# Optimization experiments

Hardware: AMD Instinct MI355X
Metric: run time of the kernel (lower is better)

## Reference

```python
import jax, jax.numpy as jnp
import numpy as np

MARGIN = 1.0


def setup_inputs() -> dict:
    key = jax.random.key(0)
    k1, k2 = jax.random.split(key)
    embeddings = jax.random.normal(k1, (4096, 512), dtype=jnp.float32)
    labels = jax.random.randint(k2, (4096,), 0, 256, dtype=jnp.int32)
    return {"embeddings": embeddings, "labels": labels}


def _masked_random_gather(dist, mask, key):
    # Uniformly sample one valid (masked-True) column per row via argmax of
    # uniform noise restricted to the mask (equivalent to torch.randint over
    # the per-row index list, fully vectorized). Rows with no valid entry -> 0.
    B = dist.shape[0]
    u = jax.random.uniform(key, mask.shape)          # [B, B] in [0, 1)
    idx = jnp.argmax(jnp.where(mask, u, -1.0), axis=1)  # [B]
    has_valid = jnp.any(mask, axis=1)
    d = dist[jnp.arange(B), idx]
    return jnp.where(has_valid, d, 0.0)


def reference(embeddings, labels):
    B = embeddings.shape[0]
    # Pairwise squared Euclidean distances: ||a||^2 + ||b||^2 - 2 a.b, clamped >= 0
    dot = embeddings @ embeddings.T                  # [B, B]
    sq = jnp.diagonal(dot)                           # [B]
    dist = jax.nn.relu(sq[None, :] + sq[:, None] - 2.0 * dot)

    same = labels[:, None] == labels[None, :]        # [B, B]
    eye = jnp.eye(B, dtype=bool)
    mask_pos = same & ~eye
    mask_neg = ~same

    kp, kn = jax.random.split(jax.random.key(42))
    positive_dist = _masked_random_gather(dist, mask_pos, kp)
    negative_dist = _masked_random_gather(dist, mask_neg, kn)

    triplet_loss = jax.nn.relu(positive_dist - negative_dist + MARGIN)
    valid = jnp.sum(triplet_loss > 1e-16)
    return jnp.where(valid == 0, jnp.float32(0.0), jnp.mean(triplet_loss))
```

## Files before the change

kernel.cpp:

```cpp
#include <hip/hip_runtime.h>
#include <stdint.h>

#define B 4096
#define D 512

#define NB_POS 16
#define NB_SQ 64
#define NB_NEG 2048
#define NB_TOTAL (NB_POS + NB_SQ + NB_NEG)

__host__ __device__ __forceinline__ uint32_t rotl32(uint32_t x, int d) {
#ifdef __HIP_DEVICE_COMPILE__
    return __builtin_amdgcn_alignbit(x, x, (uint32_t)(32 - d));
#else
    return (x << d) | (x >> (32 - d));
#endif
}

__host__ __device__ __forceinline__ void tf2x32(uint32_t k0, uint32_t k1,
                                                uint32_t x0, uint32_t x1,
                                                uint32_t& o0, uint32_t& o1) {
    const uint32_t k2 = k0 ^ k1 ^ 0x1BD11BDAu;
#define TF_ROUND(r) { x0 += x1; x1 = rotl32(x1, r); x1 ^= x0; }
    x0 += k0; x1 += k1;
    TF_ROUND(13) TF_ROUND(15) TF_ROUND(26) TF_ROUND(6)
    x0 += k1; x1 += k2 + 1u;
    TF_ROUND(17) TF_ROUND(29) TF_ROUND(16) TF_ROUND(24)
    x0 += k2; x1 += k0 + 2u;
    TF_ROUND(13) TF_ROUND(15) TF_ROUND(26) TF_ROUND(6)
    x0 += k0; x1 += k1 + 3u;
    TF_ROUND(17) TF_ROUND(29) TF_ROUND(16) TF_ROUND(24)
    x0 += k1; x1 += k2 + 4u;
    TF_ROUND(13) TF_ROUND(15) TF_ROUND(26) TF_ROUND(6)
    x0 += k2; x1 += k0 + 5u;
#undef TF_ROUND
    o0 = x0; o1 = x1;
}

__device__ __forceinline__ uint32_t draw32(uint32_t k0, uint32_t k1,
                                           uint32_t flat) {
    uint32_t o0, o1;
    tf2x32(k0, k1, 0u, flat, o0, o1);
    return o0 ^ o1;
}

__device__ __forceinline__ unsigned long long umax64(unsigned long long a,
                                                     unsigned long long b) {
    return a > b ? a : b;
}

__device__ __forceinline__ unsigned long long packbest(int bestv, int bestc) {
    return (bestv < 0)
               ? 0ull
               : ((((unsigned long long)(uint32_t)bestv + 1ull) << 12) |
                  (unsigned long long)(uint32_t)(4095 - bestc));
}

__global__ __launch_bounds__(256) void fused_select_kernel(
        const float* __restrict__ E, const int* __restrict__ labels,
        float* __restrict__ sq, int* __restrict__ idxp, int* __restrict__ idxn,
        uint32_t kp0, uint32_t kp1, uint32_t kn0, uint32_t kn1) {
    __shared__ unsigned short bposc[B];
    __shared__ int cnt[256];
    __shared__ int basex[256];
    __shared__ int fillc[256];
    __shared__ unsigned long long red[2][4];

    const int bid = blockIdx.x;
    const int t = threadIdx.x;
    const int lane = t & 63;
    const int w = t >> 6;

    if (bid >= NB_POS + NB_SQ) {
        const int r0 = (bid - (NB_POS + NB_SQ)) * 2;
        const int4* lp = (const int4*)(labels + (t << 4));
        const int4 La = lp[0], Lb = lp[1], Lc = lp[2], Ld = lp[3];
        const int lab16[16] = {La.x, La.y, La.z, La.w, Lb.x, Lb.y, Lb.z, Lb.w,
                               Lc.x, Lc.y, Lc.z, Lc.w, Ld.x, Ld.y, Ld.z, Ld.w};
        const int labr0 = labels[r0];
        const int labr1 = labels[r0 + 1];
        const uint32_t f0 = ((uint32_t)r0 << 12) + ((uint32_t)t << 4);
        int bv0 = -1, bc0 = 0, bv1 = -1, bc1 = 0;
#pragma unroll
        for (int j = 0; j < 16; ++j) {
            const int c = (t << 4) + j;
            const uint32_t h0 = draw32(kn0, kn1, f0 + (uint32_t)j);
            const uint32_t h1 = draw32(kn0, kn1, f0 + (uint32_t)j + 4096u);
            const int v0 = (int)(h0 >> 9);
            const int v1 = (int)(h1 >> 9);
            if ((lab16[j] != labr0) & (v0 > bv0)) { bv0 = v0; bc0 = c; }
            if ((lab16[j] != labr1) & (v1 > bv1)) { bv1 = v1; bc1 = c; }
        }
        unsigned long long p0 = packbest(bv0, bc0);
        unsigned long long p1 = packbest(bv1, bc1);
#pragma unroll
        for (int off = 32; off > 0; off >>= 1) {
            p0 = umax64(p0, __shfl_down(p0, off));
            p1 = umax64(p1, __shfl_down(p1, off));
        }
        if (lane == 0) { red[0][w] = p0; red[1][w] = p1; }
        __syncthreads();
        if (t < 2) {
            unsigned long long best = red[t][0];
#pragma unroll
            for (int k = 1; k < 4; ++k) best = umax64(best, red[t][k]);
            idxn[r0 + t] = best ? (int)(4095u - (uint32_t)(best & 0xFFFull))
                                : -1;
        }
    } else if (bid < NB_POS) {
        const int4* lp = (const int4*)(labels + (t << 4));
        const int4 La = lp[0], Lb = lp[1], Lc = lp[2], Ld = lp[3];
        const int lab16[16] = {La.x, La.y, La.z, La.w, Lb.x, Lb.y, Lb.z, Lb.w,
                               Lc.x, Lc.y, Lc.z, Lc.w, Ld.x, Ld.y, Ld.z, Ld.w};
        cnt[t] = 0;
        fillc[t] = 0;
        __syncthreads();
#pragma unroll
        for (int j = 0; j < 16; ++j) atomicAdd(&cnt[lab16[j]], 1);
        __syncthreads();
        basex[t] = cnt[t];
        __syncthreads();
        for (int off = 1; off < 256; off <<= 1) {
            const int u = (t >= off) ? basex[t - off] : 0;
            __syncthreads();
            basex[t] += u;
            __syncthreads();
        }
#pragma unroll
        for (int j = 0; j < 16; ++j) {
            const int l = lab16[j];
            const int off = atomicAdd(&fillc[l], 1);
            bposc[basex[l] - cnt[l] + off] = (unsigned short)((t << 4) + j);
        }
        __syncthreads();
        const int r = bid * 256 + t;
        const int myl = labels[r];
        const int s1 = basex[myl];
        const int s0 = s1 - cnt[myl];
        const uint32_t rbase = (uint32_t)r << 12;
        unsigned long long best = 0ull;
        for (int i = s0; i < s1; ++i) {
            const int c = (int)bposc[i];
            if (c == r) continue;
            const uint32_t bits = draw32(kp0, kp1, rbase + (uint32_t)c);
            const unsigned long long pack =
                ((((unsigned long long)(bits >> 9)) + 1ull) << 12) |
                (unsigned long long)(uint32_t)(4095 - c);
            best = umax64(best, pack);
        }
        idxp[r] = best ? (int)(4095u - (uint32_t)(best & 0xFFFull)) : -1;
    } else {
        const int base = (bid - NB_POS) * 64 + w * 16;
#pragma unroll 2
        for (int k = 0; k < 16; ++k) {
            const int r = base + k;
            const float4* er = (const float4*)(E + (size_t)r * D);
            float4 a0 = er[lane * 2];
            float4 a1 = er[lane * 2 + 1];
            float s = a0.x * a0.x + a0.y * a0.y + a0.z * a0.z + a0.w * a0.w +
                      a1.x * a1.x + a1.y * a1.y + a1.z * a1.z + a1.w * a1.w;
#pragma unroll
            for (int off = 32; off > 0; off >>= 1) s += __shfl_down(s, off);
            if (lane == 0) sq[r] = s;
        }
    }
}

__global__ __launch_bounds__(256) void loss_kernel(
        const float* __restrict__ E, const float* __restrict__ sq,
        const int* __restrict__ idxp, const int* __restrict__ idxn,
        float* __restrict__ tl) {
    const int lane = threadIdx.x & 63;
    const int w = threadIdx.x >> 6;
    const int r = blockIdx.x * 4 + w;
    const int ip = idxp[r];
    const int in_ = idxn[r];
    const float4* er = (const float4*)(E + (size_t)r * D);
    float dp = 0.f, dn = 0.f;
    float4 a0 = er[lane * 2];
    float4 a1 = er[lane * 2 + 1];
    if (ip >= 0) {
        const float4* ep = (const float4*)(E + (size_t)ip * D);
        float4 b0 = ep[lane * 2];
        float4 b1 = ep[lane * 2 + 1];
        dp = a0.x * b0.x + a0.y * b0.y + a0.z * b0.z + a0.w * b0.w +
             a1.x * b1.x + a1.y * b1.y + a1.z * b1.z + a1.w * b1.w;
    }
    if (in_ >= 0) {
        const float4* en = (const float4*)(E + (size_t)in_ * D);
        float4 b0 = en[lane * 2];
        float4 b1 = en[lane * 2 + 1];
        dn = a0.x * b0.x + a0.y * b0.y + a0.z * b0.z + a0.w * b0.w +
             a1.x * b1.x + a1.y * b1.y + a1.z * b1.z + a1.w * b1.w;
    }
#pragma unroll
    for (int off = 32; off > 0; off >>= 1) {
        dp += __shfl_down(dp, off);
        dn += __shfl_down(dn, off);
    }
    if (lane == 0) {
        const float pd = (ip >= 0) ? fmaxf(sq[r] + sq[ip] - 2.0f * dp, 0.f) : 0.f;
        const float nd = (in_ >= 0) ? fmaxf(sq[r] + sq[in_] - 2.0f * dn, 0.f) : 0.f;
        tl[r] = fmaxf(pd - nd + 1.0f, 0.f);
    }
}

__global__ __launch_bounds__(256) void finalize_kernel(
        const float* __restrict__ tl, float* __restrict__ out) {
    const int t = threadIdx.x;
    float s = 0.f;
    int c = 0;
    for (int j = t; j < B; j += 256) {
        const float v = tl[j];
        s += v;
        if (v > 1e-16f) c++;
    }
#pragma unroll
    for (int off = 32; off > 0; off >>= 1) {
        s += __shfl_down(s, off);
        c += __shfl_down(c, off);
    }
    __shared__ float ss[4];
    __shared__ int sc[4];
    if ((t & 63) == 0) { ss[t >> 6] = s; sc[t >> 6] = c; }
    __syncthreads();
    if (t == 0) {
#pragma unroll
        for (int k = 1; k < 4; ++k) { s += ss[k]; c += sc[k]; }
        out[0] = (c == 0) ? 0.0f : s * (1.0f / 4096.0f);
    }
}

extern "C" void kernel_launch(void* const* d_in, const int* in_sizes, int n_in,
                              void* d_out, int out_size, void* d_ws,
                              size_t ws_size, hipStream_t stream) {
    const float* E = (const float*)d_in[0];
    const int* labels = (const int*)d_in[1];
    float* out = (float*)d_out;

    char* ws = (char*)d_ws;
    float* sq = (float*)(ws);
    int* idxp = (int*)(ws + 16384);
    int* idxn = (int*)(ws + 32768);
    float* tl = (float*)(ws + 49152);

    uint32_t kp0, kp1, kn0, kn1;
    tf2x32(0u, 42u, 0u, 0u, kp0, kp1);
    tf2x32(0u, 42u, 0u, 1u, kn0, kn1);

    fused_select_kernel<<<NB_TOTAL, 256, 0, stream>>>(E, labels, sq, idxp,
                                                      idxn, kp0, kp1, kn0, kn1);
    loss_kernel<<<B / 4, 256, 0, stream>>>(E, sq, idxp, idxn, tl);
    finalize_kernel<<<1, 256, 0, stream>>>(tl, out);
}
```

Measured before the change: 50.07 us.

## Move positive selection and squared norms into loss kernel, publish label buckets

```diff
diff --git a/kernel.cpp b/kernel.cpp
--- a/kernel.cpp
+++ b/kernel.cpp
@@ -4,10 +4,7 @@
 #define B 4096
 #define D 512
 
-#define NB_POS 16
-#define NB_SQ 64
 #define NB_NEG 2048
-#define NB_TOTAL (NB_POS + NB_SQ + NB_NEG)
 
 __host__ __device__ __forceinline__ uint32_t rotl32(uint32_t x, int d) {
 #ifdef __HIP_DEVICE_COMPILE__
@@ -56,11 +53,10 @@
                   (unsigned long long)(uint32_t)(4095 - bestc));
 }
 
-__global__ __launch_bounds__(256) void fused_select_kernel(
-        const float* __restrict__ E, const int* __restrict__ labels,
-        float* __restrict__ sq, int* __restrict__ idxp, int* __restrict__ idxn,
-        uint32_t kp0, uint32_t kp1, uint32_t kn0, uint32_t kn1) {
-    __shared__ unsigned short bposc[B];
+__global__ __launch_bounds__(256) void neg_bucket_kernel(
+        const int* __restrict__ labels, int* __restrict__ idxn,
+        int* __restrict__ bstart, unsigned short* __restrict__ bcols,
+        uint32_t kn0, uint32_t kn1) {
     __shared__ int cnt[256];
     __shared__ int basex[256];
     __shared__ int fillc[256];
@@ -71,43 +67,7 @@
     const int lane = t & 63;
     const int w = t >> 6;
 
-    if (bid >= NB_POS + NB_SQ) {
-        const int r0 = (bid - (NB_POS + NB_SQ)) * 2;
-        const int4* lp = (const int4*)(labels + (t << 4));
-        const int4 La = lp[0], Lb = lp[1], Lc = lp[2], Ld = lp[3];
-        const int lab16[16] = {La.x, La.y, La.z, La.w, Lb.x, Lb.y, Lb.z, Lb.w,
-                               Lc.x, Lc.y, Lc.z, Lc.w, Ld.x, Ld.y, Ld.z, Ld.w};
-        const int labr0 = labels[r0];
-        const int labr1 = labels[r0 + 1];
-        const uint32_t f0 = ((uint32_t)r0 << 12) + ((uint32_t)t << 4);
-        int bv0 = -1, bc0 = 0, bv1 = -1, bc1 = 0;
-#pragma unroll
-        for (int j = 0; j < 16; ++j) {
-            const int c = (t << 4) + j;
-            const uint32_t h0 = draw32(kn0, kn1, f0 + (uint32_t)j);
-            const uint32_t h1 = draw32(kn0, kn1, f0 + (uint32_t)j + 4096u);
-            const int v0 = (int)(h0 >> 9);
-            const int v1 = (int)(h1 >> 9);
-            if ((lab16[j] != labr0) & (v0 > bv0)) { bv0 = v0; bc0 = c; }
-            if ((lab16[j] != labr1) & (v1 > bv1)) { bv1 = v1; bc1 = c; }
-        }
-        unsigned long long p0 = packbest(bv0, bc0);
-        unsigned long long p1 = packbest(bv1, bc1);
-#pragma unroll
-        for (int off = 32; off > 0; off >>= 1) {
-            p0 = umax64(p0, __shfl_down(p0, off));
-            p1 = umax64(p1, __shfl_down(p1, off));
-        }
-        if (lane == 0) { red[0][w] = p0; red[1][w] = p1; }
-        __syncthreads();
-        if (t < 2) {
-            unsigned long long best = red[t][0];
-#pragma unroll
-            for (int k = 1; k < 4; ++k) best = umax64(best, red[t][k]);
-            idxn[r0 + t] = best ? (int)(4095u - (uint32_t)(best & 0xFFFull))
-                                : -1;
-        }
-    } else if (bid < NB_POS) {
+    if (bid == 0) {
         const int4* lp = (const int4*)(labels + (t << 4));
         const int4 La = lp[0], Lb = lp[1], Lc = lp[2], Ld = lp[3];
         const int lab16[16] = {La.x, La.y, La.z, La.w, Lb.x, Lb.y, Lb.z, Lb.w,
@@ -126,81 +86,117 @@
             basex[t] += u;
             __syncthreads();
         }
+        bstart[t] = basex[t] - cnt[t];
+        if (t == 255) bstart[256] = B;
 #pragma unroll
         for (int j = 0; j < 16; ++j) {
             const int l = lab16[j];
             const int off = atomicAdd(&fillc[l], 1);
-            bposc[basex[l] - cnt[l] + off] = (unsigned short)((t << 4) + j);
+            bcols[basex[l] - cnt[l] + off] = (unsigned short)((t << 4) + j);
         }
         __syncthreads();
-        const int r = bid * 256 + t;
-        const int myl = labels[r];
-        const int s1 = basex[myl];
-        const int s0 = s1 - cnt[myl];
-        const uint32_t rbase = (uint32_t)r << 12;
-        unsigned long long best = 0ull;
-        for (int i = s0; i < s1; ++i) {
-            const int c = (int)bposc[i];
-            if (c == r) continue;
-            const uint32_t bits = draw32(kp0, kp1, rbase + (uint32_t)c);
-            const unsigned long long pack =
-                ((((unsigned long long)(bits >> 9)) + 1ull) << 12) |
-                (unsigned long long)(uint32_t)(4095 - c);
-            best = umax64(best, pack);
-        }
-        idxp[r] = best ? (int)(4095u - (uint32_t)(best & 0xFFFull)) : -1;
-    } else {
-        const int base = (bid - NB_POS) * 64 + w * 16;
-#pragma unroll 2
-        for (int k = 0; k < 16; ++k) {
-            const int r = base + k;
-            const float4* er = (const float4*)(E + (size_t)r * D);
-            float4 a0 = er[lane * 2];
-            float4 a1 = er[lane * 2 + 1];
-            float s = a0.x * a0.x + a0.y * a0.y + a0.z * a0.z + a0.w * a0.w +
-                      a1.x * a1.x + a1.y * a1.y + a1.z * a1.z + a1.w * a1.w;
-#pragma unroll
-            for (int off = 32; off > 0; off >>= 1) s += __shfl_down(s, off);
-            if (lane == 0) sq[r] = s;
-        }
+    }
+
+    const int r0 = bid * 2;
+    const int4* lp = (const int4*)(labels + (t << 4));
+    const int4 La = lp[0], Lb = lp[1], Lc = lp[2], Ld = lp[3];
+    const int lab16[16] = {La.x, La.y, La.z, La.w, Lb.x, Lb.y, Lb.z, Lb.w,
+                           Lc.x, Lc.y, Lc.z, Lc.w, Ld.x, Ld.y, Ld.z, Ld.w};
+    const int labr0 = labels[r0];
+    const int labr1 = labels[r0 + 1];
+    const uint32_t f0 = ((uint32_t)r0 << 12) + ((uint32_t)t << 4);
+    int bv0 = -1, bc0 = 0, bv1 = -1, bc1 = 0;
+#pragma unroll
+    for (int j = 0; j < 16; ++j) {
+        const int c = (t << 4) + j;
+        const uint32_t h0 = draw32(kn0, kn1, f0 + (uint32_t)j);
+        const uint32_t h1 = draw32(kn0, kn1, f0 + (uint32_t)j + 4096u);
+        const int v0 = (int)(h0 >> 9);
+        const int v1 = (int)(h1 >> 9);
+        if ((lab16[j] != labr0) & (v0 > bv0)) { bv0 = v0; bc0 = c; }
+        if ((lab16[j] != labr1) & (v1 > bv1)) { bv1 = v1; bc1 = c; }
+    }
+    unsigned long long p0 = packbest(bv0, bc0);
+    unsigned long long p1 = packbest(bv1, bc1);
+#pragma unroll
+    for (int off = 32; off > 0; off >>= 1) {
+        p0 = umax64(p0, __shfl_down(p0, off));
+        p1 = umax64(p1, __shfl_down(p1, off));
+    }
+    if (lane == 0) { red[0][w] = p0; red[1][w] = p1; }
+    __syncthreads();
+    if (t < 2) {
+        unsigned long long best = red[t][0];
+#pragma unroll
+        for (int k = 1; k < 4; ++k) best = umax64(best, red[t][k]);
+        idxn[r0 + t] = best ? (int)(4095u - (uint32_t)(best & 0xFFFull)) : -1;
     }
 }
 
 __global__ __launch_bounds__(256) void loss_kernel(
-        const float* __restrict__ E, const float* __restrict__ sq,
-        const int* __restrict__ idxp, const int* __restrict__ idxn,
-        float* __restrict__ tl) {
+        const float* __restrict__ E, const int* __restrict__ labels,
+        const int* __restrict__ bstart, const unsigned short* __restrict__ bcols,
+        const int* __restrict__ idxn, float* __restrict__ tl,
+        uint32_t kp0, uint32_t kp1) {
     const int lane = threadIdx.x & 63;
     const int w = threadIdx.x >> 6;
     const int r = blockIdx.x * 4 + w;
-    const int ip = idxp[r];
+
+    const int l = labels[r];
+    const int s0 = bstart[l];
+    const int s1 = bstart[l + 1];
+    const uint32_t rbase = (uint32_t)r << 12;
+    unsigned long long best = 0ull;
+    for (int i = s0 + lane; i < s1; i += 64) {
+        const int c = (int)bcols[i];
+        if (c == r) continue;
+        const uint32_t bits = draw32(kp0, kp1, rbase + (uint32_t)c);
+        const unsigned long long pack =
+            ((((unsigned long long)(bits >> 9)) + 1ull) << 12) |
+            (unsigned long long)(uint32_t)(4095 - c);
+        best = umax64(best, pack);
+    }
+#pragma unroll
+    for (int off = 32; off > 0; off >>= 1)
+        best = umax64(best, __shfl_xor(best, off));
+    const int ip = best ? (int)(4095u - (uint32_t)(best & 0xFFFull)) : -1;
     const int in_ = idxn[r];
+
     const float4* er = (const float4*)(E + (size_t)r * D);
-    float dp = 0.f, dn = 0.f;
     float4 a0 = er[lane * 2];
     float4 a1 = er[lane * 2 + 1];
+    float aa = a0.x * a0.x + a0.y * a0.y + a0.z * a0.z + a0.w * a0.w +
+               a1.x * a1.x + a1.y * a1.y + a1.z * a1.z + a1.w * a1.w;
+    float dp = 0.f, pp = 0.f, dn = 0.f, nn = 0.f;
     if (ip >= 0) {
         const float4* ep = (const float4*)(E + (size_t)ip * D);
         float4 b0 = ep[lane * 2];
         float4 b1 = ep[lane * 2 + 1];
         dp = a0.x * b0.x + a0.y * b0.y + a0.z * b0.z + a0.w * b0.w +
              a1.x * b1.x + a1.y * b1.y + a1.z * b1.z + a1.w * b1.w;
+        pp = b0.x * b0.x + b0.y * b0.y + b0.z * b0.z + b0.w * b0.w +
+             b1.x * b1.x + b1.y * b1.y + b1.z * b1.z + b1.w * b1.w;
     }
     if (in_ >= 0) {
         const float4* en = (const float4*)(E + (size_t)in_ * D);
-        float4 b0 = en[lane * 2];
-        float4 b1 = en[lane * 2 + 1];
-        dn = a0.x * b0.x + a0.y * b0.y + a0.z * b0.z + a0.w * b0.w +
-             a1.x * b1.x + a1.y * b1.y + a1.z * b1.z + a1.w * b1.w;
+        float4 c0 = en[lane * 2];
+        float4 c1 = en[lane * 2 + 1];
+        dn = a0.x * c0.x + a0.y * c0.y + a0.z * c0.z + a0.w * c0.w +
+             a1.x * c1.x + a1.y * c1.y + a1.z * c1.z + a1.w * c1.w;
+        nn = c0.x * c0.x + c0.y * c0.y + c0.z * c0.z + c0.w * c0.w +
+             c1.x * c1.x + c1.y * c1.y + c1.z * c1.z + c1.w * c1.w;
     }
 #pragma unroll
     for (int off = 32; off > 0; off >>= 1) {
+        aa += __shfl_down(aa, off);
         dp += __shfl_down(dp, off);
+        pp += __shfl_down(pp, off);
         dn += __shfl_down(dn, off);
+        nn += __shfl_down(nn, off);
     }
     if (lane == 0) {
-        const float pd = (ip >= 0) ? fmaxf(sq[r] + sq[ip] - 2.0f * dp, 0.f) : 0.f;
-        const float nd = (in_ >= 0) ? fmaxf(sq[r] + sq[in_] - 2.0f * dn, 0.f) : 0.f;
+        const float pd = (ip >= 0) ? fmaxf(aa + pp - 2.0f * dp, 0.f) : 0.f;
+        const float nd = (in_ >= 0) ? fmaxf(aa + nn - 2.0f * dn, 0.f) : 0.f;
         tl[r] = fmaxf(pd - nd + 1.0f, 0.f);
     }
 }
@@ -239,17 +235,18 @@
     float* out = (float*)d_out;
 
     char* ws = (char*)d_ws;
-    float* sq = (float*)(ws);
-    int* idxp = (int*)(ws + 16384);
-    int* idxn = (int*)(ws + 32768);
-    float* tl = (float*)(ws + 49152);
+    int* idxn = (int*)(ws);
+    float* tl = (float*)(ws + 16384);
+    int* bstart = (int*)(ws + 32768);
+    unsigned short* bcols = (unsigned short*)(ws + 36864);
 
     uint32_t kp0, kp1, kn0, kn1;
     tf2x32(0u, 42u, 0u, 0u, kp0, kp1);
     tf2x32(0u, 42u, 0u, 1u, kn0, kn1);
 
-    fused_select_kernel<<<NB_TOTAL, 256, 0, stream>>>(E, labels, sq, idxp,
-                                                      idxn, kp0, kp1, kn0, kn1);
-    loss_kernel<<<B / 4, 256, 0, stream>>>(E, sq, idxp, idxn, tl);
+    neg_bucket_kernel<<<NB_NEG, 256, 0, stream>>>(labels, idxn, bstart, bcols,
+                                                  kn0, kn1);
+    loss_kernel<<<B / 4, 256, 0, stream>>>(E, labels, bstart, bcols, idxn, tl,
+                                           kp0, kp1);
     finalize_kernel<<<1, 256, 0, stream>>>(tl, out);
 }
```

Result: faster. 47.23 us, median of 2 (-5.7%).
